# Kernel tuning notes

Measured on AMD Instinct MI355X. Metric: run time of the kernel, lower is better.

Reference implementation:

```python
import jax, jax.numpy as jnp
import numpy as np
import math

E = 1024   # embed_dim
H = 16     # num_heads
D = E // H # head_dim


def _rotary(x):
    # x: [B, H, S, D]. Faithful to the original quirky implementation:
    # pos_enc[:, 0::2] = sin(position * div_term), then cos/sin are taken OF that value.
    S = x.shape[2]
    position = jnp.arange(S, dtype=jnp.float32)[:, None]                     # [S,1]
    div_term = jnp.exp(jnp.arange(0, D, 2, dtype=jnp.float32) * (-math.log(10000.0) / D))  # [D/2]
    angle = jnp.sin(position * div_term)                                     # [S, D/2] == pos_enc[:,0::2]
    cos_t = jnp.cos(angle)                                                   # [S, D/2]
    sin_t = jnp.sin(angle)                                                   # [S, D/2]
    xe = x[..., 0::2]
    xo = x[..., 1::2]
    re = xe * cos_t - xo * sin_t
    ro = xo * cos_t + xe * sin_t
    # interleave even/odd back: [..., D/2, 2] -> [..., D]
    return jnp.stack([re, ro], axis=-1).reshape(x.shape)


def setup_inputs() -> dict:
    key = jax.random.key(0)
    ks = jax.random.split(key, 12)
    B, S = 4, 1024
    scale = 1.0 / math.sqrt(E)
    inp = {
        "query": jax.random.normal(ks[0], (B, S, E), dtype=jnp.float32),
        "key":   jax.random.normal(ks[1], (B, S, E), dtype=jnp.float32),
        "value": jax.random.normal(ks[2], (B, S, E), dtype=jnp.float32),
        # Linear params stored as [in, out]; y = x @ W + b
        "Wq": jax.random.normal(ks[3], (E, E), dtype=jnp.float32) * scale,
        "bq": jnp.zeros((E,), dtype=jnp.float32),
        "Wk": jax.random.normal(ks[4], (E, E), dtype=jnp.float32) * scale,
        "bk": jnp.zeros((E,), dtype=jnp.float32),
        "Wv": jax.random.normal(ks[5], (E, E), dtype=jnp.float32) * scale,
        "bv": jnp.zeros((E,), dtype=jnp.float32),
        "Wo": jax.random.normal(ks[6], (E, E), dtype=jnp.float32) * scale,
        "bo": jnp.zeros((E,), dtype=jnp.float32),
    }
    return inp


def reference(query, key, value, Wq, bq, Wk, bk, Wv, bv, Wo, bo):
    B, S, _ = query.shape
    # projections -> [B, H, S, D]
    q = (query @ Wq + bq).reshape(B, S, H, D).transpose(0, 2, 1, 3)
    k = (key   @ Wk + bk).reshape(B, S, H, D).transpose(0, 2, 1, 3)
    v = (value @ Wv + bv).reshape(B, S, H, D).transpose(0, 2, 1, 3)
    q = _rotary(q)
    k = _rotary(k)
    scores = jnp.einsum('bhsd,bhtd->bhst', q, k) / (D ** 0.5)  # [B,H,S,S]
    probs = jax.nn.softmax(scores, axis=-1)
    # dropout p=0 (eval) -> identity
    ctx = jnp.einsum('bhst,bhtd->bhsd', probs, v)              # [B,H,S,D]
    ctx = ctx.transpose(0, 2, 1, 3).reshape(B, S, E)
    out = ctx @ Wo + bo
    return out, probs
```

## Files before the change

### kernel.cpp

```cpp
#include <hip/hip_runtime.h>
#include <hip/hip_bf16.h>

typedef __attribute__((ext_vector_type(8))) short bf16x8;
typedef __attribute__((ext_vector_type(4))) float f32x4;
typedef unsigned short u16;

__device__ __forceinline__ u16 f2bf(float f) {
  unsigned u = __float_as_uint(f);
  u += 0x7fffu + ((u >> 16) & 1u);
  return (u16)(u >> 16);
}

__device__ __forceinline__ void gload16(const void* g, void* l) {
  __builtin_amdgcn_global_load_lds(
      (const __attribute__((address_space(1))) unsigned int*)g,
      (__attribute__((address_space(3))) unsigned int*)l, 16, 0, 0);
}

__global__ __launch_bounds__(256) void prep_kernel(
    const float* __restrict__ query, const float* __restrict__ key_,
    const float* __restrict__ value, u16* __restrict__ qin,
    u16* __restrict__ kin, u16* __restrict__ vin,
    const float* __restrict__ Wq, const float* __restrict__ Wk,
    const float* __restrict__ Wv, const float* __restrict__ Wo,
    u16* __restrict__ WqT, u16* __restrict__ WkT, u16* __restrict__ WvT,
    u16* __restrict__ WoT, float* __restrict__ cosT, float* __restrict__ sinT) {
  __shared__ float tile[32][33];
  const int z = blockIdx.z;
  const int bx = blockIdx.x;
  const int tid = threadIdx.x;
  if (z < 3) {
    const float* in = z == 0 ? query : z == 1 ? key_ : value;
    u16* out = z == 0 ? qin : z == 1 ? kin : vin;
    size_t i = ((size_t)bx * 256 + tid) * 4;
    float4 v = *(const float4*)(in + i);
    ushort4 o = make_ushort4(f2bf(v.x), f2bf(v.y), f2bf(v.z), f2bf(v.w));
    *(ushort4*)(out + i) = o;
  } else if (z == 3) {
    const int w = bx >> 10;
    const float* W = w == 0 ? Wq : w == 1 ? Wk : w == 2 ? Wv : Wo;
    u16* Wt = w == 0 ? WqT : w == 1 ? WkT : w == 2 ? WvT : WoT;
    int tx = tid & 31, ty = tid >> 5;
    int k0 = ((bx >> 5) & 31) * 32, n0 = (bx & 31) * 32;
#pragma unroll
    for (int i = 0; i < 4; ++i)
      tile[ty + i * 8][tx] = W[(size_t)(k0 + ty + i * 8) * 1024 + n0 + tx];
    __syncthreads();
#pragma unroll
    for (int i = 0; i < 4; ++i)
      Wt[(size_t)(n0 + ty + i * 8) * 1024 + k0 + tx] = f2bf(tile[tx][ty + i * 8]);
  } else {
    int i = bx * 256 + tid;
    if (i >= 1024 * 32) return;
    int s = i >> 5, p = i & 31;
    double freq = exp(-9.210340371976184 * (double)(2 * p) / 64.0);
    double ang = sin((double)s * freq);
    cosT[i] = (float)cos(ang);
    sinT[i] = (float)sin(ang);
  }
}

__global__ __launch_bounds__(256) void vtrans_kernel(const u16* __restrict__ vb,
                                                     u16* __restrict__ vt) {
  __shared__ u16 tile[64][72];
  int z = blockIdx.y, b = z >> 4, h = z & 15;
  int s0 = blockIdx.x * 64;
  int t = threadIdx.x;
#pragma unroll
  for (int it = 0; it < 2; ++it) {
    int idx = t + it * 256;
    int s = idx >> 3, d = (idx & 7) * 8;
    bf16x8 v = *(const bf16x8*)(vb + ((size_t)(b * 1024 + s0 + s) * 1024 + h * 64 + d));
    *(bf16x8*)&tile[s][d] = v;
  }
  __syncthreads();
#pragma unroll
  for (int it = 0; it < 2; ++it) {
    int idx = t + it * 256;
    int d = idx >> 3, sc = (idx & 7) * 8;
    bf16x8 o;
#pragma unroll
    for (int i = 0; i < 8; ++i) o[i] = (short)tile[sc + i][d];
    *(bf16x8*)(vt + ((size_t)(z * 64 + d)) * 1024 + s0 + sc) = o;
  }
}

__global__ __launch_bounds__(256) void proj_gemm_kernel(
    const u16* __restrict__ qin, const u16* __restrict__ kin,
    const u16* __restrict__ vin, const u16* __restrict__ WqT,
    const u16* __restrict__ WkT, const u16* __restrict__ WvT,
    const float* __restrict__ bq, const float* __restrict__ bk,
    const float* __restrict__ bv, u16* __restrict__ qr, u16* __restrict__ kr,
    u16* __restrict__ vb, const float* __restrict__ cosT,
    const float* __restrict__ sinT) {
  __shared__ u16 lA[128 * 32];
  __shared__ u16 lB[128 * 32];
  const int z = blockIdx.z;
  const u16* A = z == 0 ? qin : z == 1 ? kin : vin;
  const u16* Bt = z == 0 ? WqT : z == 1 ? WkT : WvT;
  const float* bias = z == 0 ? bq : z == 1 ? bk : bv;
  u16* Cout = z == 0 ? qr : z == 1 ? kr : vb;

  const int tid = threadIdx.x;
  const int lane = tid & 63, wid = tid >> 6;
  const int wm = wid >> 1, wn = wid & 1;
  const int lr = lane & 15, kg = lane >> 4;
  const int m0 = blockIdx.y * 128, n0 = blockIdx.x * 128;

  f32x4 acc[4][4] = {};
  for (int k0 = 0; k0 < 1024; k0 += 32) {
#pragma unroll
    for (int it = 0; it < 2; ++it) {
      int o = tid * 16 + it * 4096;
      int row = o >> 6;
      int cbs = (((o >> 4) & 3) ^ (row & 3)) << 4;
      gload16((const char*)A + ((size_t)(m0 + row) * 1024 + k0) * 2 + cbs, (char*)lA + o);
      gload16((const char*)Bt + ((size_t)(n0 + row) * 1024 + k0) * 2 + cbs, (char*)lB + o);
    }
    __syncthreads();
    bf16x8 av[4], bv_[4];
#pragma unroll
    for (int i = 0; i < 4; ++i) {
      int ra = wm * 64 + i * 16 + lr;
      av[i] = *(const bf16x8*)((const char*)lA + ra * 64 + ((kg ^ (ra & 3)) << 4));
      int rb = wn * 64 + i * 16 + lr;
      bv_[i] = *(const bf16x8*)((const char*)lB + rb * 64 + ((kg ^ (rb & 3)) << 4));
    }
#pragma unroll
    for (int i = 0; i < 4; ++i)
#pragma unroll
      for (int j = 0; j < 4; ++j)
        acc[i][j] = __builtin_amdgcn_mfma_f32_16x16x32_bf16(av[i], bv_[j], acc[i][j], 0, 0, 0);
    __syncthreads();
  }
#pragma unroll
  for (int i = 0; i < 4; ++i) {
#pragma unroll
    for (int j = 0; j < 4; ++j) {
      int col = n0 + wn * 64 + j * 16 + lr;
      float bcol = bias[col];
#pragma unroll
      for (int r = 0; r < 4; ++r) {
        int row = m0 + wm * 64 + i * 16 + kg * 4 + r;
        float v = acc[i][j][r] + bcol;
        if (z == 2) {
          Cout[(size_t)row * 1024 + col] = f2bf(v);
        } else {
          float pv = __shfl_xor(v, 1);
          int p = (col & 63) >> 1;
          int s = row & 1023;
          float ct = cosT[s * 32 + p], st = sinT[s * 32 + p];
          float ov = (col & 1) ? (v * ct + pv * st) : (v * ct - pv * st);
          Cout[(size_t)row * 1024 + col] = f2bf(ov);
        }
      }
    }
  }
}

__global__ __launch_bounds__(256) void out_gemm_kernel(
    const u16* __restrict__ A, const u16* __restrict__ Bt,
    const float* __restrict__ bias, float* __restrict__ Cout) {
  __shared__ u16 lA[128 * 32];
  __shared__ u16 lB[128 * 32];
  const int tid = threadIdx.x;
  const int lane = tid & 63, wid = tid >> 6;
  const int wm = wid >> 1, wn = wid & 1;
  const int lr = lane & 15, kg = lane >> 4;
  const int m0 = blockIdx.y * 128, n0 = blockIdx.x * 128;

  f32x4 acc[4][4] = {};
  for (int k0 = 0; k0 < 1024; k0 += 32) {
#pragma unroll
    for (int it = 0; it < 2; ++it) {
      int o = tid * 16 + it * 4096;
      int row = o >> 6;
      int cbs = (((o >> 4) & 3) ^ (row & 3)) << 4;
      gload16((const char*)A + ((size_t)(m0 + row) * 1024 + k0) * 2 + cbs, (char*)lA + o);
      gload16((const char*)Bt + ((size_t)(n0 + row) * 1024 + k0) * 2 + cbs, (char*)lB + o);
    }
    __syncthreads();
    bf16x8 av[4], bv_[4];
#pragma unroll
    for (int i = 0; i < 4; ++i) {
      int ra = wm * 64 + i * 16 + lr;
      av[i] = *(const bf16x8*)((const char*)lA + ra * 64 + ((kg ^ (ra & 3)) << 4));
      int rb = wn * 64 + i * 16 + lr;
      bv_[i] = *(const bf16x8*)((const char*)lB + rb * 64 + ((kg ^ (rb & 3)) << 4));
    }
#pragma unroll
    for (int i = 0; i < 4; ++i)
#pragma unroll
      for (int j = 0; j < 4; ++j)
        acc[i][j] = __builtin_amdgcn_mfma_f32_16x16x32_bf16(av[i], bv_[j], acc[i][j], 0, 0, 0);
    __syncthreads();
  }
#pragma unroll
  for (int i = 0; i < 4; ++i)
#pragma unroll
    for (int j = 0; j < 4; ++j) {
      int col = n0 + wn * 64 + j * 16 + lr;
      float bcol = bias[col];
#pragma unroll
      for (int r = 0; r < 4; ++r) {
        int row = m0 + wm * 64 + i * 16 + kg * 4 + r;
        Cout[(size_t)row * 1024 + col] = acc[i][j][r] + bcol;
      }
    }
}

__global__ __launch_bounds__(256, 2) void fused_attn_kernel(
    const u16* __restrict__ qr, const u16* __restrict__ kr,
    const u16* __restrict__ vt, float* __restrict__ probs,
    u16* __restrict__ ctx) {
  __shared__ u16 lQ[32 * 64];
  __shared__ u16 lK[2][128 * 64];
  __shared__ u16 lV[2][64 * 128];
  __shared__ u16 lP[32 * 128];
  __shared__ float redM[4][32];
  __shared__ float redS[4][32];

  const int tid = threadIdx.x;
  const int lane = tid & 63, wid = tid >> 6;
  const int lr = lane & 15, kg = lane >> 4;
  const int z = blockIdx.y, b = z >> 4, h = z & 15;
  const int m0 = blockIdx.x * 32;

  const char* Qb = (const char*)qr + ((size_t)(b * 1024 + m0) * 1024 + h * 64) * 2;
  const char* Kb = (const char*)kr + ((size_t)(b * 1024) * 1024 + h * 64) * 2;
  const char* Vb = (const char*)vt + (size_t)z * 64 * 1024 * 2;

  {
    int o = tid * 16;
    int row = o >> 7, ch = (o >> 4) & 7;
    gload16(Qb + (size_t)row * 2048 + ((ch ^ (row & 7)) << 4), (char*)lQ + o);
  }
#pragma unroll
  for (int it = 0; it < 4; ++it) {
    int o = tid * 16 + it * 4096;
    int row = o >> 7, ch = (o >> 4) & 7;
    gload16(Kb + (size_t)row * 2048 + ((ch ^ (row & 7)) << 4), (char*)lK[0] + o);
  }
  __syncthreads();

  bf16x8 qf[2][2];
#pragma unroll
  for (int ii = 0; ii < 2; ++ii)
#pragma unroll
    for (int ks = 0; ks < 2; ++ks) {
      int ra = ii * 16 + lr;
      int cc = ks * 4 + kg;
      qf[ii][ks] = *(const bf16x8*)((const char*)lQ + ra * 128 + ((cc ^ (ra & 7)) << 4));
    }

  f32x4 accS[8][2][2] = {};
#pragma unroll
  for (int c = 0; c < 8; ++c) {
    if (c < 7) {
#pragma unroll
      for (int it = 0; it < 4; ++it) {
        int o = tid * 16 + it * 4096;
        int row = o >> 7, ch = (o >> 4) & 7;
        gload16(Kb + (size_t)((c + 1) * 128 + row) * 2048 + ((ch ^ (row & 7)) << 4),
                (char*)lK[(c + 1) & 1] + o);
      }
    }
#pragma unroll
    for (int ks = 0; ks < 2; ++ks) {
      bf16x8 bvf[2];
#pragma unroll
      for (int jj = 0; jj < 2; ++jj) {
        int rb = wid * 32 + jj * 16 + lr;
        int cc = ks * 4 + kg;
        bvf[jj] = *(const bf16x8*)((const char*)lK[c & 1] + rb * 128 + ((cc ^ (rb & 7)) << 4));
      }
#pragma unroll
      for (int ii = 0; ii < 2; ++ii)
#pragma unroll
        for (int jj = 0; jj < 2; ++jj)
          accS[c][ii][jj] =
              __builtin_amdgcn_mfma_f32_16x16x32_bf16(qf[ii][ks], bvf[jj], accS[c][ii][jj], 0, 0, 0);
    }
    __syncthreads();
  }

#pragma unroll
  for (int it = 0; it < 4; ++it) {
    int o = tid * 16 + it * 4096;
    int row = o >> 8, ch = (o >> 4) & 15;
    gload16(Vb + (size_t)row * 2048 + ((ch ^ (row & 15)) << 4), (char*)lV[0] + o);
  }

  float rmax[2][4];
#pragma unroll
  for (int ii = 0; ii < 2; ++ii)
#pragma unroll
    for (int r = 0; r < 4; ++r) rmax[ii][r] = -1e30f;
#pragma unroll
  for (int c = 0; c < 8; ++c)
#pragma unroll
    for (int ii = 0; ii < 2; ++ii)
#pragma unroll
      for (int jj = 0; jj < 2; ++jj)
#pragma unroll
        for (int r = 0; r < 4; ++r) {
          float v = accS[c][ii][jj][r] * 0.125f;
          accS[c][ii][jj][r] = v;
          rmax[ii][r] = fmaxf(rmax[ii][r], v);
        }
#pragma unroll
  for (int ii = 0; ii < 2; ++ii)
#pragma unroll
    for (int r = 0; r < 4; ++r) {
      float v = rmax[ii][r];
      v = fmaxf(v, __shfl_xor(v, 1));
      v = fmaxf(v, __shfl_xor(v, 2));
      v = fmaxf(v, __shfl_xor(v, 4));
      v = fmaxf(v, __shfl_xor(v, 8));
      rmax[ii][r] = v;
    }
  if (lr == 0) {
#pragma unroll
    for (int ii = 0; ii < 2; ++ii)
#pragma unroll
      for (int r = 0; r < 4; ++r) redM[wid][ii * 16 + kg * 4 + r] = rmax[ii][r];
  }
  __syncthreads();
  float rowm[2][4], rsum[2][4];
#pragma unroll
  for (int ii = 0; ii < 2; ++ii)
#pragma unroll
    for (int r = 0; r < 4; ++r) {
      int row = ii * 16 + kg * 4 + r;
      rowm[ii][r] = fmaxf(fmaxf(redM[0][row], redM[1][row]), fmaxf(redM[2][row], redM[3][row]));
      rsum[ii][r] = 0.f;
    }
#pragma unroll
  for (int c = 0; c < 8; ++c)
#pragma unroll
    for (int ii = 0; ii < 2; ++ii)
#pragma unroll
      for (int jj = 0; jj < 2; ++jj)
#pragma unroll
        for (int r = 0; r < 4; ++r) {
          float e = __expf(accS[c][ii][jj][r] - rowm[ii][r]);
          accS[c][ii][jj][r] = e;
          rsum[ii][r] += e;
        }
#pragma unroll
  for (int ii = 0; ii < 2; ++ii)
#pragma unroll
    for (int r = 0; r < 4; ++r) {
      float v = rsum[ii][r];
      v += __shfl_xor(v, 1);
      v += __shfl_xor(v, 2);
      v += __shfl_xor(v, 4);
      v += __shfl_xor(v, 8);
      rsum[ii][r] = v;
    }
  if (lr == 0) {
#pragma unroll
    for (int ii = 0; ii < 2; ++ii)
#pragma unroll
      for (int r = 0; r < 4; ++r) redS[wid][ii * 16 + kg * 4 + r] = rsum[ii][r];
  }
  __syncthreads();
  float inv[2][4];
#pragma unroll
  for (int ii = 0; ii < 2; ++ii)
#pragma unroll
    for (int r = 0; r < 4; ++r) {
      int row = ii * 16 + kg * 4 + r;
      inv[ii][r] = 1.0f / (redS[0][row] + redS[1][row] + redS[2][row] + redS[3][row]);
    }

  const int ipv = wid >> 1, jpv = wid & 1;
  f32x4 accPV[2] = {};
  float* Pg = probs + (size_t)z * 1024 * 1024 + (size_t)m0 * 1024;

#pragma unroll
  for (int c = 0; c < 8; ++c) {
#pragma unroll
    for (int ii = 0; ii < 2; ++ii)
#pragma unroll
      for (int jj = 0; jj < 2; ++jj)
#pragma unroll
        for (int r = 0; r < 4; ++r) {
          float p = accS[c][ii][jj][r] * inv[ii][r];
          int row = ii * 16 + kg * 4 + r;
          int col = wid * 32 + jj * 16 + lr;
          Pg[(size_t)row * 1024 + c * 128 + col] = p;
          *(u16*)((char*)lP + row * 256 + ((((col >> 3) ^ (row & 15))) << 4) + (col & 7) * 2) =
              f2bf(p);
        }
    if (c < 7) {
#pragma unroll
      for (int it = 0; it < 4; ++it) {
        int o = tid * 16 + it * 4096;
        int row = o >> 8, ch = (o >> 4) & 15;
        gload16(Vb + (size_t)row * 2048 + (c + 1) * 256 + ((ch ^ (row & 15)) << 4),
                (char*)lV[(c + 1) & 1] + o);
      }
    }
    __syncthreads();
#pragma unroll
    for (int ks = 0; ks < 4; ++ks) {
      int cc = ks * 4 + kg;
      int ra = ipv * 16 + lr;
      bf16x8 pa = *(const bf16x8*)((const char*)lP + ra * 256 + ((cc ^ (ra & 15)) << 4));
#pragma unroll
      for (int jjj = 0; jjj < 2; ++jjj) {
        int rb = jpv * 32 + jjj * 16 + lr;
        bf16x8 vbf = *(const bf16x8*)((const char*)lV[c & 1] + rb * 256 + ((cc ^ (rb & 15)) << 4));
        accPV[jjj] = __builtin_amdgcn_mfma_f32_16x16x32_bf16(pa, vbf, accPV[jjj], 0, 0, 0);
      }
    }
    __syncthreads();
  }

#pragma unroll
  for (int jjj = 0; jjj < 2; ++jjj)
#pragma unroll
    for (int r = 0; r < 4; ++r) {
      int row = m0 + ipv * 16 + kg * 4 + r;
      int d = jpv * 32 + jjj * 16 + lr;
      ctx[((size_t)(b * 1024 + row)) * 1024 + h * 64 + d] = f2bf(accPV[jjj][r]);
    }
}

extern "C" void kernel_launch(void* const* d_in, const int* in_sizes, int n_in,
                              void* d_out, int out_size, void* d_ws, size_t ws_size,
                              hipStream_t stream) {
  const float* query = (const float*)d_in[0];
  const float* key_ = (const float*)d_in[1];
  const float* value = (const float*)d_in[2];
  const float* Wq = (const float*)d_in[3];
  const float* bq = (const float*)d_in[4];
  const float* Wk = (const float*)d_in[5];
  const float* bk = (const float*)d_in[6];
  const float* Wv = (const float*)d_in[7];
  const float* bv = (const float*)d_in[8];
  const float* Wo = (const float*)d_in[9];
  const float* bo = (const float*)d_in[10];

  float* out = (float*)d_out;
  float* probs = out + (size_t)4 * 1024 * 1024;

  char* w = (char*)d_ws;
  const size_t SZ_MK = (size_t)4096 * 1024 * 2;
  const size_t SZ_W = (size_t)1024 * 1024 * 2;
  u16* qin = (u16*)w; w += SZ_MK;
  u16* kin = (u16*)w; w += SZ_MK;
  u16* vin = (u16*)w; w += SZ_MK;
  u16* qr = (u16*)w; w += SZ_MK;
  u16* kr = (u16*)w; w += SZ_MK;
  u16* vb = (u16*)w; w += SZ_MK;
  u16* WqT = (u16*)w; w += SZ_W;
  u16* WkT = (u16*)w; w += SZ_W;
  u16* WvT = (u16*)w; w += SZ_W;
  u16* WoT = (u16*)w; w += SZ_W;
  float* cosT = (float*)w; w += 1024 * 32 * 4;
  float* sinT = (float*)w; w += 1024 * 32 * 4;
  u16* vt = kin;
  u16* ctx = qin;

  dim3 blk(256);
  hipLaunchKernelGGL(prep_kernel, dim3(4096, 1, 5), blk, 0, stream,
                     query, key_, value, qin, kin, vin, Wq, Wk, Wv, Wo,
                     WqT, WkT, WvT, WoT, cosT, sinT);
  hipLaunchKernelGGL(proj_gemm_kernel, dim3(8, 32, 3), blk, 0, stream,
                     qin, kin, vin, WqT, WkT, WvT, bq, bk, bv, qr, kr, vb,
                     cosT, sinT);
  hipLaunchKernelGGL(vtrans_kernel, dim3(16, 64), blk, 0, stream, vb, vt);
  hipLaunchKernelGGL(fused_attn_kernel, dim3(32, 64), blk, 0, stream,
                     qr, kr, vt, probs, ctx);
  hipLaunchKernelGGL(out_gemm_kernel, dim3(8, 32), blk, 0, stream,
                     ctx, WoT, bo, out);
}
```

Before: 190.2 us.

## Double-buffer GEMM loads, fuse V transpose into projection, pipeline attention loads

```diff
diff --git a/kernel.cpp b/kernel.cpp
--- a/kernel.cpp
+++ b/kernel.cpp
@@ -15,6 +15,12 @@
   __builtin_amdgcn_global_load_lds(
       (const __attribute__((address_space(1))) unsigned int*)g,
       (__attribute__((address_space(3))) unsigned int*)l, 16, 0, 0);
+}
+
+__device__ __forceinline__ void blockbar() {
+  asm volatile("" ::: "memory");
+  __builtin_amdgcn_s_barrier();
+  asm volatile("" ::: "memory");
 }
 
 __global__ __launch_bounds__(256) void prep_kernel(
@@ -60,46 +66,20 @@
   }
 }
 
-__global__ __launch_bounds__(256) void vtrans_kernel(const u16* __restrict__ vb,
-                                                     u16* __restrict__ vt) {
-  __shared__ u16 tile[64][72];
-  int z = blockIdx.y, b = z >> 4, h = z & 15;
-  int s0 = blockIdx.x * 64;
-  int t = threadIdx.x;
-#pragma unroll
-  for (int it = 0; it < 2; ++it) {
-    int idx = t + it * 256;
-    int s = idx >> 3, d = (idx & 7) * 8;
-    bf16x8 v = *(const bf16x8*)(vb + ((size_t)(b * 1024 + s0 + s) * 1024 + h * 64 + d));
-    *(bf16x8*)&tile[s][d] = v;
-  }
-  __syncthreads();
-#pragma unroll
-  for (int it = 0; it < 2; ++it) {
-    int idx = t + it * 256;
-    int d = idx >> 3, sc = (idx & 7) * 8;
-    bf16x8 o;
-#pragma unroll
-    for (int i = 0; i < 8; ++i) o[i] = (short)tile[sc + i][d];
-    *(bf16x8*)(vt + ((size_t)(z * 64 + d)) * 1024 + s0 + sc) = o;
-  }
-}
-
 __global__ __launch_bounds__(256) void proj_gemm_kernel(
     const u16* __restrict__ qin, const u16* __restrict__ kin,
     const u16* __restrict__ vin, const u16* __restrict__ WqT,
     const u16* __restrict__ WkT, const u16* __restrict__ WvT,
     const float* __restrict__ bq, const float* __restrict__ bk,
     const float* __restrict__ bv, u16* __restrict__ qr, u16* __restrict__ kr,
-    u16* __restrict__ vb, const float* __restrict__ cosT,
+    u16* __restrict__ vt, const float* __restrict__ cosT,
     const float* __restrict__ sinT) {
-  __shared__ u16 lA[128 * 32];
-  __shared__ u16 lB[128 * 32];
+  __shared__ u16 lA[2][128 * 32];
+  __shared__ u16 lB[2][128 * 32];
   const int z = blockIdx.z;
   const u16* A = z == 0 ? qin : z == 1 ? kin : vin;
   const u16* Bt = z == 0 ? WqT : z == 1 ? WkT : WvT;
   const float* bias = z == 0 ? bq : z == 1 ? bk : bv;
-  u16* Cout = z == 0 ? qr : z == 1 ? kr : vb;
 
   const int tid = threadIdx.x;
   const int lane = tid & 63, wid = tid >> 6;
@@ -107,45 +87,76 @@
   const int lr = lane & 15, kg = lane >> 4;
   const int m0 = blockIdx.y * 128, n0 = blockIdx.x * 128;
 
-  f32x4 acc[4][4] = {};
-  for (int k0 = 0; k0 < 1024; k0 += 32) {
+  auto stage = [&](int bu, int k0) {
 #pragma unroll
     for (int it = 0; it < 2; ++it) {
       int o = tid * 16 + it * 4096;
       int row = o >> 6;
       int cbs = (((o >> 4) & 3) ^ (row & 3)) << 4;
-      gload16((const char*)A + ((size_t)(m0 + row) * 1024 + k0) * 2 + cbs, (char*)lA + o);
-      gload16((const char*)Bt + ((size_t)(n0 + row) * 1024 + k0) * 2 + cbs, (char*)lB + o);
-    }
-    __syncthreads();
+      gload16((const char*)A + ((size_t)(m0 + row) * 1024 + k0) * 2 + cbs,
+              (char*)lA[bu] + o);
+      gload16((const char*)Bt + ((size_t)(n0 + row) * 1024 + k0) * 2 + cbs,
+              (char*)lB[bu] + o);
+    }
+  };
+
+  stage(0, 0);
+  f32x4 acc[4][4] = {};
+  for (int t = 0; t < 32; ++t) {
+    if (t < 31) {
+      stage((t + 1) & 1, (t + 1) * 32);
+      asm volatile("s_waitcnt vmcnt(4)" ::: "memory");
+    } else {
+      asm volatile("s_waitcnt vmcnt(0)" ::: "memory");
+    }
+    blockbar();
+    const int cb = t & 1;
     bf16x8 av[4], bv_[4];
 #pragma unroll
     for (int i = 0; i < 4; ++i) {
       int ra = wm * 64 + i * 16 + lr;
-      av[i] = *(const bf16x8*)((const char*)lA + ra * 64 + ((kg ^ (ra & 3)) << 4));
+      av[i] = *(const bf16x8*)((const char*)lA[cb] + ra * 64 + ((kg ^ (ra & 3)) << 4));
       int rb = wn * 64 + i * 16 + lr;
-      bv_[i] = *(const bf16x8*)((const char*)lB + rb * 64 + ((kg ^ (rb & 3)) << 4));
+      bv_[i] = *(const bf16x8*)((const char*)lB[cb] + rb * 64 + ((kg ^ (rb & 3)) << 4));
     }
 #pragma unroll
     for (int i = 0; i < 4; ++i)
 #pragma unroll
       for (int j = 0; j < 4; ++j)
         acc[i][j] = __builtin_amdgcn_mfma_f32_16x16x32_bf16(av[i], bv_[j], acc[i][j], 0, 0, 0);
-    __syncthreads();
-  }
-#pragma unroll
-  for (int i = 0; i < 4; ++i) {
-#pragma unroll
-    for (int j = 0; j < 4; ++j) {
-      int col = n0 + wn * 64 + j * 16 + lr;
-      float bcol = bias[col];
-#pragma unroll
-      for (int r = 0; r < 4; ++r) {
-        int row = m0 + wm * 64 + i * 16 + kg * 4 + r;
-        float v = acc[i][j][r] + bcol;
-        if (z == 2) {
-          Cout[(size_t)row * 1024 + col] = f2bf(v);
-        } else {
+    blockbar();
+  }
+
+  if (z == 2) {
+    const int bb = m0 >> 10;
+#pragma unroll
+    for (int i = 0; i < 4; ++i) {
+      int srow = (m0 & 1023) + wm * 64 + i * 16 + kg * 4;
+#pragma unroll
+      for (int j = 0; j < 4; ++j) {
+        int col = n0 + wn * 64 + j * 16 + lr;
+        float bcol = bias[col];
+        int h = col >> 6, d = col & 63;
+        ushort4 o;
+        o.x = f2bf(acc[i][j][0] + bcol);
+        o.y = f2bf(acc[i][j][1] + bcol);
+        o.z = f2bf(acc[i][j][2] + bcol);
+        o.w = f2bf(acc[i][j][3] + bcol);
+        *(ushort4*)(vt + ((size_t)((bb * 16 + h) * 64 + d)) * 1024 + srow) = o;
+      }
+    }
+  } else {
+    u16* Cout = z == 0 ? qr : kr;
+#pragma unroll
+    for (int i = 0; i < 4; ++i) {
+#pragma unroll
+      for (int j = 0; j < 4; ++j) {
+        int col = n0 + wn * 64 + j * 16 + lr;
+        float bcol = bias[col];
+#pragma unroll
+        for (int r = 0; r < 4; ++r) {
+          int row = m0 + wm * 64 + i * 16 + kg * 4 + r;
+          float v = acc[i][j][r] + bcol;
           float pv = __shfl_xor(v, 1);
           int p = (col & 63) >> 1;
           int s = row & 1023;
@@ -161,39 +172,52 @@
 __global__ __launch_bounds__(256) void out_gemm_kernel(
     const u16* __restrict__ A, const u16* __restrict__ Bt,
     const float* __restrict__ bias, float* __restrict__ Cout) {
-  __shared__ u16 lA[128 * 32];
-  __shared__ u16 lB[128 * 32];
+  __shared__ u16 lA[2][128 * 32];
+  __shared__ u16 lB[2][128 * 32];
   const int tid = threadIdx.x;
   const int lane = tid & 63, wid = tid >> 6;
   const int wm = wid >> 1, wn = wid & 1;
   const int lr = lane & 15, kg = lane >> 4;
   const int m0 = blockIdx.y * 128, n0 = blockIdx.x * 128;
 
-  f32x4 acc[4][4] = {};
-  for (int k0 = 0; k0 < 1024; k0 += 32) {
+  auto stage = [&](int bu, int k0) {
 #pragma unroll
     for (int it = 0; it < 2; ++it) {
       int o = tid * 16 + it * 4096;
       int row = o >> 6;
       int cbs = (((o >> 4) & 3) ^ (row & 3)) << 4;
-      gload16((const char*)A + ((size_t)(m0 + row) * 1024 + k0) * 2 + cbs, (char*)lA + o);
-      gload16((const char*)Bt + ((size_t)(n0 + row) * 1024 + k0) * 2 + cbs, (char*)lB + o);
-    }
-    __syncthreads();
+      gload16((const char*)A + ((size_t)(m0 + row) * 1024 + k0) * 2 + cbs,
+              (char*)lA[bu] + o);
+      gload16((const char*)Bt + ((size_t)(n0 + row) * 1024 + k0) * 2 + cbs,
+              (char*)lB[bu] + o);
+    }
+  };
+
+  stage(0, 0);
+  f32x4 acc[4][4] = {};
+  for (int t = 0; t < 32; ++t) {
+    if (t < 31) {
+      stage((t + 1) & 1, (t + 1) * 32);
+      asm volatile("s_waitcnt vmcnt(4)" ::: "memory");
+    } else {
+      asm volatile("s_waitcnt vmcnt(0)" ::: "memory");
+    }
+    blockbar();
+    const int cb = t & 1;
     bf16x8 av[4], bv_[4];
 #pragma unroll
     for (int i = 0; i < 4; ++i) {
       int ra = wm * 64 + i * 16 + lr;
-      av[i] = *(const bf16x8*)((const char*)lA + ra * 64 + ((kg ^ (ra & 3)) << 4));
+      av[i] = *(const bf16x8*)((const char*)lA[cb] + ra * 64 + ((kg ^ (ra & 3)) << 4));
       int rb = wn * 64 + i * 16 + lr;
-      bv_[i] = *(const bf16x8*)((const char*)lB + rb * 64 + ((kg ^ (rb & 3)) << 4));
+      bv_[i] = *(const bf16x8*)((const char*)lB[cb] + rb * 64 + ((kg ^ (rb & 3)) << 4));
     }
 #pragma unroll
     for (int i = 0; i < 4; ++i)
 #pragma unroll
       for (int j = 0; j < 4; ++j)
         acc[i][j] = __builtin_amdgcn_mfma_f32_16x16x32_bf16(av[i], bv_[j], acc[i][j], 0, 0, 0);
-    __syncthreads();
+    blockbar();
   }
 #pragma unroll
   for (int i = 0; i < 4; ++i)
@@ -230,40 +254,52 @@
   const char* Kb = (const char*)kr + ((size_t)(b * 1024) * 1024 + h * 64) * 2;
   const char* Vb = (const char*)vt + (size_t)z * 64 * 1024 * 2;
 
+  auto stageK = [&](int bu, int c) {
+#pragma unroll
+    for (int it = 0; it < 4; ++it) {
+      int o = tid * 16 + it * 4096;
+      int row = o >> 7, ch = (o >> 4) & 7;
+      gload16(Kb + (size_t)(c * 128 + row) * 2048 + ((ch ^ (row & 7)) << 4),
+              (char*)lK[bu] + o);
+    }
+  };
+  auto stageV = [&](int bu, int c) {
+#pragma unroll
+    for (int it = 0; it < 4; ++it) {
+      int o = tid * 16 + it * 4096;
+      int row = o >> 8, ch = (o >> 4) & 15;
+      gload16(Vb + (size_t)row * 2048 + c * 256 + ((ch ^ (row & 15)) << 4),
+              (char*)lV[bu] + o);
+    }
+  };
+
   {
     int o = tid * 16;
     int row = o >> 7, ch = (o >> 4) & 7;
     gload16(Qb + (size_t)row * 2048 + ((ch ^ (row & 7)) << 4), (char*)lQ + o);
   }
-#pragma unroll
-  for (int it = 0; it < 4; ++it) {
-    int o = tid * 16 + it * 4096;
-    int row = o >> 7, ch = (o >> 4) & 7;
-    gload16(Kb + (size_t)row * 2048 + ((ch ^ (row & 7)) << 4), (char*)lK[0] + o);
-  }
-  __syncthreads();
+  stageK(0, 0);
 
   bf16x8 qf[2][2];
-#pragma unroll
-  for (int ii = 0; ii < 2; ++ii)
-#pragma unroll
-    for (int ks = 0; ks < 2; ++ks) {
-      int ra = ii * 16 + lr;
-      int cc = ks * 4 + kg;
-      qf[ii][ks] = *(const bf16x8*)((const char*)lQ + ra * 128 + ((cc ^ (ra & 7)) << 4));
-    }
-
   f32x4 accS[8][2][2] = {};
 #pragma unroll
   for (int c = 0; c < 8; ++c) {
     if (c < 7) {
-#pragma unroll
-      for (int it = 0; it < 4; ++it) {
-        int o = tid * 16 + it * 4096;
-        int row = o >> 7, ch = (o >> 4) & 7;
-        gload16(Kb + (size_t)((c + 1) * 128 + row) * 2048 + ((ch ^ (row & 7)) << 4),
-                (char*)lK[(c + 1) & 1] + o);
-      }
+      stageK((c + 1) & 1, c + 1);
+      asm volatile("s_waitcnt vmcnt(4)" ::: "memory");
+    } else {
+      asm volatile("s_waitcnt vmcnt(0)" ::: "memory");
+    }
+    blockbar();
+    if (c == 0) {
+#pragma unroll
+      for (int ii = 0; ii < 2; ++ii)
+#pragma unroll
+        for (int ks = 0; ks < 2; ++ks) {
+          int ra = ii * 16 + lr;
+          int cc = ks * 4 + kg;
+          qf[ii][ks] = *(const bf16x8*)((const char*)lQ + ra * 128 + ((cc ^ (ra & 7)) << 4));
+        }
     }
 #pragma unroll
     for (int ks = 0; ks < 2; ++ks) {
@@ -281,15 +317,10 @@
           accS[c][ii][jj] =
               __builtin_amdgcn_mfma_f32_16x16x32_bf16(qf[ii][ks], bvf[jj], accS[c][ii][jj], 0, 0, 0);
     }
-    __syncthreads();
-  }
-
-#pragma unroll
-  for (int it = 0; it < 4; ++it) {
-    int o = tid * 16 + it * 4096;
-    int row = o >> 8, ch = (o >> 4) & 15;
-    gload16(Vb + (size_t)row * 2048 + ((ch ^ (row & 15)) << 4), (char*)lV[0] + o);
-  }
+    blockbar();
+  }
+
+  stageV(0, 0);
 
   float rmax[2][4];
 #pragma unroll
@@ -325,7 +356,8 @@
 #pragma unroll
       for (int r = 0; r < 4; ++r) redM[wid][ii * 16 + kg * 4 + r] = rmax[ii][r];
   }
-  __syncthreads();
+  asm volatile("s_waitcnt lgkmcnt(0)" ::: "memory");
+  blockbar();
   float rowm[2][4], rsum[2][4];
 #pragma unroll
   for (int ii = 0; ii < 2; ++ii)
@@ -364,7 +396,8 @@
 #pragma unroll
       for (int r = 0; r < 4; ++r) redS[wid][ii * 16 + kg * 4 + r] = rsum[ii][r];
   }
-  __syncthreads();
+  asm volatile("s_waitcnt lgkmcnt(0)" ::: "memory");
+  blockbar();
   float inv[2][4];
 #pragma unroll
   for (int ii = 0; ii < 2; ++ii)
@@ -380,6 +413,7 @@
 
 #pragma unroll
   for (int c = 0; c < 8; ++c) {
+    if (c < 7) stageV((c + 1) & 1, c + 1);
 #pragma unroll
     for (int ii = 0; ii < 2; ++ii)
 #pragma unroll
@@ -393,16 +427,11 @@
           *(u16*)((char*)lP + row * 256 + ((((col >> 3) ^ (row & 15))) << 4) + (col & 7) * 2) =
               f2bf(p);
         }
-    if (c < 7) {
-#pragma unroll
-      for (int it = 0; it < 4; ++it) {
-        int o = tid * 16 + it * 4096;
-        int row = o >> 8, ch = (o >> 4) & 15;
-        gload16(Vb + (size_t)row * 2048 + (c + 1) * 256 + ((ch ^ (row & 15)) << 4),
-                (char*)lV[(c + 1) & 1] + o);
-      }
-    }
-    __syncthreads();
+    if (c < 7)
+      asm volatile("s_waitcnt vmcnt(20) lgkmcnt(0)" ::: "memory");
+    else
+      asm volatile("s_waitcnt vmcnt(16) lgkmcnt(0)" ::: "memory");
+    blockbar();
 #pragma unroll
     for (int ks = 0; ks < 4; ++ks) {
       int cc = ks * 4 + kg;
@@ -415,7 +444,7 @@
         accPV[jjj] = __builtin_amdgcn_mfma_f32_16x16x32_bf16(pa, vbf, accPV[jjj], 0, 0, 0);
       }
     }
-    __syncthreads();
+    blockbar();
   }
 
 #pragma unroll
@@ -454,14 +483,13 @@
   u16* vin = (u16*)w; w += SZ_MK;
   u16* qr = (u16*)w; w += SZ_MK;
   u16* kr = (u16*)w; w += SZ_MK;
-  u16* vb = (u16*)w; w += SZ_MK;
+  u16* vt = (u16*)w; w += SZ_MK;
   u16* WqT = (u16*)w; w += SZ_W;
   u16* WkT = (u16*)w; w += SZ_W;
   u16* WvT = (u16*)w; w += SZ_W;
   u16* WoT = (u16*)w; w += SZ_W;
   float* cosT = (float*)w; w += 1024 * 32 * 4;
   float* sinT = (float*)w; w += 1024 * 32 * 4;
-  u16* vt = kin;
   u16* ctx = qin;
 
   dim3 blk(256);
@@ -469,9 +497,8 @@
                      query, key_, value, qin, kin, vin, Wq, Wk, Wv, Wo,
                      WqT, WkT, WvT, WoT, cosT, sinT);
   hipLaunchKernelGGL(proj_gemm_kernel, dim3(8, 32, 3), blk, 0, stream,
-                     qin, kin, vin, WqT, WkT, WvT, bq, bk, bv, qr, kr, vb,
+                     qin, kin, vin, WqT, WkT, WvT, bq, bk, bv, qr, kr, vt,
                      cosT, sinT);
-  hipLaunchKernelGGL(vtrans_kernel, dim3(16, 64), blk, 0, stream, vb, vt);
   hipLaunchKernelGGL(fused_attn_kernel, dim3(32, 64), blk, 0, stream,
                      qr, kr, vt, probs, ctx);
   hipLaunchKernelGGL(out_gemm_kernel, dim3(8, 32), blk, 0, stream,
```

New measurement: 189.1 us. No clear change (-0.6%).
